# Optimization experiments

Hardware: AMD Instinct MI355X
Metric: run time of the kernel (lower is better)

Reference implementation:

```python
import jax, jax.numpy as jnp
import numpy as np

T = 256  # max number of words (segments) per sentence

def _pool_one(h, wid):
    # h: [S, H], wid: [S] int32 in [0, T)
    sums = jax.ops.segment_sum(h, wid, num_segments=T)              # [T, H]
    counts = jax.ops.segment_sum(jnp.ones(h.shape[0], h.dtype), wid, num_segments=T)  # [T]
    # torch: mean over empty group -> NaN -> nan_to_num -> 0
    return jnp.where(counts[:, None] > 0, sums / jnp.maximum(counts, 1.0)[:, None], 0.0)

def setup_inputs() -> dict:
    key = jax.random.key(0)
    k1, k2, k3, k4, k5 = jax.random.split(key, 5)
    B, S, H, E = 64, 512, 768, 512
    hidden_states = jax.random.normal(k1, (B, S, H), dtype=jnp.float32)
    word_ids = jnp.sort(jax.random.randint(k2, (B, S), 0, T, dtype=jnp.int32), axis=-1)
    token_lengths = jax.random.randint(k3, (B,), 1, T + 1, dtype=jnp.int32)
    W = jax.random.normal(k4, (E, H), dtype=jnp.float32) / np.sqrt(H)
    b = jax.random.normal(k5, (E,), dtype=jnp.float32) * 0.02
    return {"hidden_states": hidden_states, "word_ids": word_ids,
            "token_lengths": token_lengths, "W": W, "b": b}

def reference(hidden_states, word_ids, token_lengths, W, b):
    # masked segment-mean pooling: [B, S, H] -> [B, T, H]
    pooled = jax.vmap(_pool_one)(hidden_states, word_ids)
    # zero out word slots beyond token_lengths[i] (original only fills _id < token_lengths[i])
    mask = jnp.arange(T)[None, :] < token_lengths[:, None]          # [B, T]
    pooled = jnp.where(mask[:, :, None], pooled, 0.0)
    # linear projection (bias applied everywhere, matching nn.Linear on zero rows)
    return jnp.einsum("bth,eh->bte", pooled, W) + b
```

## Files before the change

kernel.cpp:

```cpp
#include <hip/hip_runtime.h>


#define B_N   64
#define S_LEN 512
#define H_DIM 768
#define E_DIM 512
#define T_SEG 256
#define M_TOT (B_N * T_SEG)

typedef unsigned short u16;
typedef __bf16 bf16x8 __attribute__((ext_vector_type(8)));
typedef float f32x4 __attribute__((ext_vector_type(4)));

__device__ __forceinline__ u16 f2bf(float x) {
    union { float f; unsigned int u; } v; v.f = x;
    unsigned int r = (v.u + 0x7fffu + ((v.u >> 16) & 1u)) >> 16;
    return (u16)r;
}

__global__ __launch_bounds__(256) void prep_kernel(
    const float* __restrict__ W, u16* __restrict__ Wbf,
    const int* __restrict__ wid, int* __restrict__ starts, int* __restrict__ counts) {
    __shared__ int cnt[T_SEG];
    const int tid = threadIdx.x;
    if (blockIdx.x < 384) {
        const int i = (blockIdx.x * 256 + tid) * 4;
        const float4 f = *reinterpret_cast<const float4*>(W + i);
        ushort4 u;
        u.x = f2bf(f.x); u.y = f2bf(f.y); u.z = f2bf(f.z); u.w = f2bf(f.w);
        *reinterpret_cast<ushort4*>(Wbf + i) = u;
        return;
    }
    const int b = blockIdx.x - 384;
    cnt[tid] = 0;
    __syncthreads();
    {
        const int s0 = wid[b * S_LEN + tid];
        const int s1 = wid[b * S_LEN + 256 + tid];
        atomicAdd(&cnt[s0], 1);
        atomicAdd(&cnt[s1], 1);
    }
    __syncthreads();
    const int v = cnt[tid];
    for (int off = 1; off < T_SEG; off <<= 1) {
        int t = 0;
        if (tid >= off) t = cnt[tid - off];
        __syncthreads();
        cnt[tid] += t;
        __syncthreads();
    }
    starts[b * T_SEG + tid] = cnt[tid] - v;
    counts[b * T_SEG + tid] = v;
}

__global__ __launch_bounds__(192) void pool_kernel(
    const float* __restrict__ hidden, const int* __restrict__ tlen,
    const int* __restrict__ starts, const int* __restrict__ counts,
    u16* __restrict__ pooled) {
    const int t = blockIdx.x, b = blockIdx.y, tid = threadIdx.x;
    const int idx = b * T_SEG + t;
    const int cnt = counts[idx];
    const int st  = starts[idx];
    const bool live = (t < tlen[b]) && (cnt > 0);
    f32x4 a0 = {0.f, 0.f, 0.f, 0.f}, a1 = {0.f, 0.f, 0.f, 0.f};
    if (live) {
        const f32x4* base = reinterpret_cast<const f32x4*>(
            hidden + (size_t)(b * S_LEN + st) * H_DIM) + tid;
        int s = 0;
        for (; s + 2 <= cnt; s += 2) {
            a0 += base[0];
            a1 += base[192];
            base += 384;
        }
        if (s < cnt) a0 += base[0];
        a0 += a1;
        const float inv = 1.0f / (float)cnt;
        a0 *= inv;
    }
    ushort4 u;
    u.x = f2bf(a0[0]); u.y = f2bf(a0[1]); u.z = f2bf(a0[2]); u.w = f2bf(a0[3]);
    *reinterpret_cast<ushort4*>(pooled + (size_t)idx * H_DIM + tid * 4) = u;
}

__global__ __launch_bounds__(256) void gemm_bt_kernel(
    const u16* __restrict__ A, const u16* __restrict__ Bm,
    const float* __restrict__ bias, float* __restrict__ C) {
    constexpr int BM = 128, BN = 128, BK = 64, K = H_DIM, N = E_DIM;
    __shared__ u16 lA[BM * BK];
    __shared__ u16 lB[BN * BK];

    const int tid  = threadIdx.x;
    const int wave = tid >> 6;
    const int lane = tid & 63;
    const int wm = wave >> 1, wn = wave & 1;
    const int m0 = blockIdx.x * BM;
    const int n0 = blockIdx.y * BN;

    const int lrow = lane >> 3;
    const int lcol = (lane & 7) * 8;

    f32x4 acc[4][4] = {};

    for (int k0 = 0; k0 < K; k0 += BK) {
#pragma unroll
        for (int i = 0; i < 4; ++i) {
            const int c = wave * 4 + i;
            const int row = c * 8 + lrow;
            const u16* ga = A  + (size_t)(m0 + row) * K + k0 + lcol;
            const u16* gb = Bm + (size_t)(n0 + row) * K + k0 + lcol;
            __builtin_amdgcn_global_load_lds(
                (const __attribute__((address_space(1))) void*)ga,
                (__attribute__((address_space(3))) void*)(lA + c * 512), 16, 0, 0);
            __builtin_amdgcn_global_load_lds(
                (const __attribute__((address_space(1))) void*)gb,
                (__attribute__((address_space(3))) void*)(lB + c * 512), 16, 0, 0);
        }
        __syncthreads();

#pragma unroll
        for (int kt = 0; kt < 2; ++kt) {
            const int ko = kt * 32 + (lane >> 4) * 8;
            bf16x8 af[4], bfv[4];
#pragma unroll
            for (int i = 0; i < 4; ++i) {
                const int ar = wm * 64 + i * 16 + (lane & 15);
                af[i]  = *reinterpret_cast<const bf16x8*>(lA + ar * BK + ko);
                const int br = wn * 64 + i * 16 + (lane & 15);
                bfv[i] = *reinterpret_cast<const bf16x8*>(lB + br * BK + ko);
            }
#pragma unroll
            for (int mi = 0; mi < 4; ++mi)
#pragma unroll
                for (int ni = 0; ni < 4; ++ni)
                    acc[mi][ni] = __builtin_amdgcn_mfma_f32_16x16x32_bf16(
                        af[mi], bfv[ni], acc[mi][ni], 0, 0, 0);
        }
        __syncthreads();
    }

    const int cn = lane & 15;
    const int rq = (lane >> 4) * 4;
#pragma unroll
    for (int ni = 0; ni < 4; ++ni) {
        const int gn = n0 + wn * 64 + ni * 16 + cn;
        const float bv = bias[gn];
#pragma unroll
        for (int mi = 0; mi < 4; ++mi) {
            const int gmb = m0 + wm * 64 + mi * 16 + rq;
#pragma unroll
            for (int r = 0; r < 4; ++r)
                C[(size_t)(gmb + r) * N + gn] = acc[mi][ni][r] + bv;
        }
    }
}

extern "C" void kernel_launch(void* const* d_in, const int* in_sizes, int n_in,
                              void* d_out, int out_size, void* d_ws, size_t ws_size,
                              hipStream_t stream) {
    const float* hidden = (const float*)d_in[0];
    const int*   wid    = (const int*)d_in[1];
    const int*   tlen   = (const int*)d_in[2];
    const float* W      = (const float*)d_in[3];
    const float* bias   = (const float*)d_in[4];
    float* out = (float*)d_out;

    constexpr size_t POOLED_BYTES = (size_t)M_TOT * H_DIM * 2;
    constexpr size_t WBF_BYTES    = (size_t)E_DIM * H_DIM * 2;
    constexpr size_t SC_BYTES     = (size_t)B_N * T_SEG * 4;
    char* ws = (char*)d_ws;
    u16* pooled = (u16*)ws;
    u16* wbf    = (u16*)(ws + POOLED_BYTES);
    int* starts = (int*)(ws + POOLED_BYTES + WBF_BYTES);
    int* counts = (int*)(ws + POOLED_BYTES + WBF_BYTES + SC_BYTES);

    prep_kernel<<<448, 256, 0, stream>>>(W, wbf, wid, starts, counts);
    pool_kernel<<<dim3(T_SEG, B_N), 192, 0, stream>>>(hidden, tlen, starts, counts, pooled);
    gemm_bt_kernel<<<dim3(M_TOT / 128, E_DIM / 128), 256, 0, stream>>>(pooled, wbf, bias, out);
}
```

Baseline: 177.4 us.

## Fuse segment-boundary computation into pooling and skip GEMM tiles beyond token length

Removes the separate prep kernel. Each pool block now finds its segment start and count with wave ballots and popcounts over the sorted word ids, and the W-to-bf16 conversion is folded into the same launch, cutting one kernel launch and the starts/counts workspace round trip. Pool blocks in the upper half whose sentence length is at most 128 exit early without writing. The GEMM writes only bias for 128-row tiles that lie entirely past the token length, skipping their MFMA work. The pool blocks now run 256 threads with 64 idle during accumulation, and each block rereads the 512 word ids.

```diff
diff --git a/kernel.cpp b/kernel.cpp
--- a/kernel.cpp
+++ b/kernel.cpp
@@ -7,6 +7,8 @@
 #define E_DIM 512
 #define T_SEG 256
 #define M_TOT (B_N * T_SEG)
+#define POOL_BLOCKS M_TOT
+#define WCONV_BLOCKS ((E_DIM * H_DIM) / 1024)
 
 typedef unsigned short u16;
 typedef __bf16 bf16x8 __attribute__((ext_vector_type(8)));
@@ -18,52 +20,46 @@
     return (u16)r;
 }
 
-__global__ __launch_bounds__(256) void prep_kernel(
-    const float* __restrict__ W, u16* __restrict__ Wbf,
-    const int* __restrict__ wid, int* __restrict__ starts, int* __restrict__ counts) {
-    __shared__ int cnt[T_SEG];
+__global__ __launch_bounds__(256) void pool_or_wconv_kernel(
+    const float* __restrict__ hidden, const int* __restrict__ wid,
+    const int* __restrict__ tlen, const float* __restrict__ W,
+    u16* __restrict__ wbf, u16* __restrict__ pooled) {
     const int tid = threadIdx.x;
-    if (blockIdx.x < 384) {
-        const int i = (blockIdx.x * 256 + tid) * 4;
+
+    if (blockIdx.x >= POOL_BLOCKS) {
+        const int i = ((blockIdx.x - POOL_BLOCKS) * 256 + tid) * 4;
         const float4 f = *reinterpret_cast<const float4*>(W + i);
         ushort4 u;
         u.x = f2bf(f.x); u.y = f2bf(f.y); u.z = f2bf(f.z); u.w = f2bf(f.w);
-        *reinterpret_cast<ushort4*>(Wbf + i) = u;
+        *reinterpret_cast<ushort4*>(wbf + i) = u;
         return;
     }
-    const int b = blockIdx.x - 384;
-    cnt[tid] = 0;
-    __syncthreads();
-    {
-        const int s0 = wid[b * S_LEN + tid];
-        const int s1 = wid[b * S_LEN + 256 + tid];
-        atomicAdd(&cnt[s0], 1);
-        atomicAdd(&cnt[s1], 1);
+
+    const int b = blockIdx.x >> 8;
+    const int t = blockIdx.x & 255;
+    const int tl = tlen[b];
+
+    if (t >= 128 && tl <= 128) return;
+
+    const int w0 = wid[b * S_LEN + tid];
+    const int w1 = wid[b * S_LEN + 256 + tid];
+    const unsigned long long blt0 = __ballot(w0 < t);
+    const unsigned long long blt1 = __ballot(w1 < t);
+    const unsigned long long beq0 = __ballot(w0 == t);
+    const unsigned long long beq1 = __ballot(w1 == t);
+    __shared__ int red[8];
+    const int wave = tid >> 6, lane = tid & 63;
+    if (lane == 0) {
+        red[wave]     = __popcll(blt0) + __popcll(blt1);
+        red[4 + wave] = __popcll(beq0) + __popcll(beq1);
     }
     __syncthreads();
-    const int v = cnt[tid];
-    for (int off = 1; off < T_SEG; off <<= 1) {
-        int t = 0;
-        if (tid >= off) t = cnt[tid - off];
-        __syncthreads();
-        cnt[tid] += t;
-        __syncthreads();
-    }
-    starts[b * T_SEG + tid] = cnt[tid] - v;
-    counts[b * T_SEG + tid] = v;
-}
+    const int st  = red[0] + red[1] + red[2] + red[3];
+    const int cnt = red[4] + red[5] + red[6] + red[7];
 
-__global__ __launch_bounds__(192) void pool_kernel(
-    const float* __restrict__ hidden, const int* __restrict__ tlen,
-    const int* __restrict__ starts, const int* __restrict__ counts,
-    u16* __restrict__ pooled) {
-    const int t = blockIdx.x, b = blockIdx.y, tid = threadIdx.x;
-    const int idx = b * T_SEG + t;
-    const int cnt = counts[idx];
-    const int st  = starts[idx];
-    const bool live = (t < tlen[b]) && (cnt > 0);
+    const bool live = (t < tl) && (cnt > 0);
     f32x4 a0 = {0.f, 0.f, 0.f, 0.f}, a1 = {0.f, 0.f, 0.f, 0.f};
-    if (live) {
+    if (live && tid < 192) {
         const f32x4* base = reinterpret_cast<const f32x4*>(
             hidden + (size_t)(b * S_LEN + st) * H_DIM) + tid;
         int s = 0;
@@ -77,24 +73,42 @@
         const float inv = 1.0f / (float)cnt;
         a0 *= inv;
     }
-    ushort4 u;
-    u.x = f2bf(a0[0]); u.y = f2bf(a0[1]); u.z = f2bf(a0[2]); u.w = f2bf(a0[3]);
-    *reinterpret_cast<ushort4*>(pooled + (size_t)idx * H_DIM + tid * 4) = u;
+    if (tid < 192) {
+        ushort4 u;
+        u.x = f2bf(a0[0]); u.y = f2bf(a0[1]); u.z = f2bf(a0[2]); u.w = f2bf(a0[3]);
+        *reinterpret_cast<ushort4*>(
+            pooled + (size_t)(blockIdx.x) * H_DIM + tid * 4) = u;
+    }
 }
 
 __global__ __launch_bounds__(256) void gemm_bt_kernel(
     const u16* __restrict__ A, const u16* __restrict__ Bm,
-    const float* __restrict__ bias, float* __restrict__ C) {
+    const float* __restrict__ bias, const int* __restrict__ tlen,
+    float* __restrict__ C) {
     constexpr int BM = 128, BN = 128, BK = 64, K = H_DIM, N = E_DIM;
     __shared__ u16 lA[BM * BK];
     __shared__ u16 lB[BN * BK];
 
     const int tid  = threadIdx.x;
+    const int m0 = blockIdx.x * BM;
+    const int n0 = blockIdx.y * BN;
+
+    const int bb = m0 >> 8;
+    const int t0 = m0 & 255;
+    if (t0 >= tlen[bb]) {
+        const float4 bv = *reinterpret_cast<const float4*>(bias + n0 + (tid & 31) * 4);
+        float* base = C + (size_t)m0 * N + n0;
+#pragma unroll
+        for (int it = 0; it < 16; ++it) {
+            const int row = it * 8 + (tid >> 5);
+            *reinterpret_cast<float4*>(base + (size_t)row * N + (tid & 31) * 4) = bv;
+        }
+        return;
+    }
+
     const int wave = tid >> 6;
     const int lane = tid & 63;
     const int wm = wave >> 1, wn = wave & 1;
-    const int m0 = blockIdx.x * BM;
-    const int n0 = blockIdx.y * BN;
 
     const int lrow = lane >> 3;
     const int lcol = (lane & 7) * 8;
@@ -165,15 +179,12 @@
     float* out = (float*)d_out;
 
     constexpr size_t POOLED_BYTES = (size_t)M_TOT * H_DIM * 2;
-    constexpr size_t WBF_BYTES    = (size_t)E_DIM * H_DIM * 2;
-    constexpr size_t SC_BYTES     = (size_t)B_N * T_SEG * 4;
     char* ws = (char*)d_ws;
     u16* pooled = (u16*)ws;
     u16* wbf    = (u16*)(ws + POOLED_BYTES);
-    int* starts = (int*)(ws + POOLED_BYTES + WBF_BYTES);
-    int* counts = (int*)(ws + POOLED_BYTES + WBF_BYTES + SC_BYTES);
 
-    prep_kernel<<<448, 256, 0, stream>>>(W, wbf, wid, starts, counts);
-    pool_kernel<<<dim3(T_SEG, B_N), 192, 0, stream>>>(hidden, tlen, starts, counts, pooled);
-    gemm_bt_kernel<<<dim3(M_TOT / 128, E_DIM / 128), 256, 0, stream>>>(pooled, wbf, bias, out);
+    pool_or_wconv_kernel<<<POOL_BLOCKS + WCONV_BLOCKS, 256, 0, stream>>>(
+        hidden, wid, tlen, W, wbf, pooled);
+    gemm_bt_kernel<<<dim3(M_TOT / 128, E_DIM / 128), 256, 0, stream>>>(
+        pooled, wbf, bias, tlen, out);
 }
```

Result: faster. 172.7 us, median of 2 (-2.7%).
